# Performance work log

Measured on AMD Instinct MI355X. Metric: run time of the kernel, lower is better.

Reference implementation:

```python
import jax, jax.numpy as jnp
import numpy as np

B, CIN, T, H, W = 2, 256, 16, 16, 8
FF, COUT, NHEADS = 512, 256, 8
TEMP = 16.0
BN_EPS = 1e-5


def setup_inputs() -> dict:
    key = jax.random.key(0)
    ks = jax.random.split(key, 6)
    s_in = 1.0 / np.sqrt(CIN)
    s_ff = 1.0 / np.sqrt(FF)
    return {
        "x": jax.random.normal(ks[0], (B, CIN, T, H, W), jnp.float32),
        "WK": jax.random.uniform(ks[1], (FF, CIN), jnp.float32, -s_in, s_in),
        "WQ": jax.random.uniform(ks[2], (FF, CIN), jnp.float32, -s_in, s_in),
        "WV": jax.random.uniform(ks[3], (FF, CIN), jnp.float32, -s_in, s_in),
        "Wo": jax.random.uniform(ks[4], (COUT, FF), jnp.float32, -s_ff, s_ff),
        "bo": jax.random.uniform(ks[5], (COUT,), jnp.float32, -s_ff, s_ff),
        "gamma": jnp.ones((COUT,), jnp.float32),
        "beta": jnp.zeros((COUT,), jnp.float32),
    }


def reference(x, WK, WQ, WV, Wo, bo, gamma, beta):
    N = T * H * W
    xf = x.reshape(B, CIN, N)  # 1x1 conv3d == channel matmul
    dh = FF // NHEADS
    K = jnp.einsum("fc,bcn->bfn", WK, xf).reshape(B, NHEADS, dh, N)
    Q = jnp.einsum("fc,bcn->bfn", WQ, xf).reshape(B, NHEADS, dh, N)
    V = jnp.einsum("fc,bcn->bfn", WV, xf).reshape(B, NHEADS, dh, N)
    # KQ[b,h,i,j] = K_i . Q_j  (i = key token, j = query token, as in torch)
    KQ = jnp.einsum("bhdi,bhdj->bhij", K, Q) / TEMP
    # block-causal mask: token time index t = token_idx // (H*W); tril -> allow i >= j
    t_idx = jnp.arange(N) // (H * W)
    allow = t_idx[:, None] >= t_idx[None, :]  # (N, N)
    KQ = jnp.where(allow[None, None], KQ, -jnp.inf)
    attn = jax.nn.softmax(KQ, axis=3)  # softmax over j (last dim), as in torch
    # out[b,h,d,i] = sum_j V[b,h,d,j] * attn[b,h,i,j]
    Vo = jnp.einsum("bhdj,bhij->bhdi", V, attn).reshape(B, FF, N)
    y = jnp.einsum("of,bfn->bon", Wo, Vo) + bo[None, :, None]
    y = jax.nn.relu(y).reshape(B, COUT, T, H, W)
    out = x + y  # skip: out_dim == in_dim
    # BatchNorm3d (training-mode batch stats, biased var)
    mean = out.mean(axis=(0, 2, 3, 4), keepdims=True)
    var = out.var(axis=(0, 2, 3, 4), keepdims=True)
    norm = (out - mean) * jax.lax.rsqrt(var + BN_EPS)
    return norm * gamma[None, :, None, None, None] + beta[None, :, None, None, None]
```

## Files before the change

kernel.cpp:

```cpp
#include <hip/hip_runtime.h>
#include <math.h>

#define BB_   2
#define CIN_  256
#define NTOK_ 2048
#define FF_   512
#define COUT_ 256
#define NH_   8
#define DH_   64
#define HW_   128
#define BNEPS_ 1e-5f
#define SCALE_LOG2_ 0.09016844005556021f

typedef __attribute__((ext_vector_type(8))) short short8;
typedef __attribute__((ext_vector_type(4))) short bfx4;
typedef __attribute__((ext_vector_type(4))) float f32x4;

#if __has_builtin(__builtin_amdgcn_mfma_f32_16x16x16_bf16)
#define MFMA16(a, b, c) __builtin_amdgcn_mfma_f32_16x16x16_bf16(a, b, c, 0, 0, 0)
#else
#define MFMA16(a, b, c) __builtin_amdgcn_mfma_f32_16x16x16bf16_1k(a, b, c, 0, 0, 0)
#endif

__device__ inline unsigned short f2bf(float f) {
  union { float f; unsigned u; } v; v.f = f;
  unsigned r = (v.u + 0x7FFF + ((v.u >> 16) & 1)) >> 16;
  return (unsigned short)r;
}

__device__ __forceinline__ void dma16(const unsigned short* g, unsigned short* l) {
  __builtin_amdgcn_global_load_lds(
      (const __attribute__((address_space(1))) void*)g,
      (__attribute__((address_space(3))) void*)l, 16, 0, 0);
}

__global__ __launch_bounds__(256) void prep_kernel(
    const float* __restrict__ x, const float* __restrict__ WK,
    const float* __restrict__ WQ, const float* __restrict__ WV,
    const float* __restrict__ Wo, unsigned short* __restrict__ xT,
    unsigned short* __restrict__ Wkb, unsigned short* __restrict__ Wqb,
    unsigned short* __restrict__ Wvb, unsigned short* __restrict__ Wob) {
  __shared__ float T[64 * 65];
  const int tid = threadIdx.x;
  const int bid = blockIdx.x;
  if (bid < 256) {
    const int b = bid >> 7;
    const int rem = bid & 127;
    const int n0 = (rem >> 2) * 64;
    const int c0 = (rem & 3) * 64;
#pragma unroll
    for (int p = 0; p < 4; ++p) {
      const int idx = tid + 256 * p;
      const int row = idx >> 4, col = (idx & 15) * 4;
      const float4 v =
          *(const float4*)(x + (size_t)(b * CIN_ + c0 + row) * NTOK_ + n0 + col);
      T[row * 65 + col + 0] = v.x; T[row * 65 + col + 1] = v.y;
      T[row * 65 + col + 2] = v.z; T[row * 65 + col + 3] = v.w;
    }
    __syncthreads();
#pragma unroll
    for (int p = 0; p < 2; ++p) {
      const int idx = tid + 256 * p;
      const int nl = idx >> 3, c8 = (idx & 7) * 8;
      unsigned short u[8];
#pragma unroll
      for (int i = 0; i < 8; ++i) u[i] = f2bf(T[(c8 + i) * 65 + nl]);
      *(uint4*)(xT + ((size_t)(b * NTOK_ + n0 + nl)) * CIN_ + c0 + c8) =
          *(uint4*)u;
    }
  } else {
    const int t = bid - 256;
    const int which = t >> 5, blk = t & 31;
    const float* src = which == 0 ? WK : which == 1 ? WQ : which == 2 ? WV : Wo;
    unsigned short* dst = which == 0 ? Wkb : which == 1 ? Wqb : which == 2 ? Wvb : Wob;
    const int base = blk * 4096 + tid * 16;
#pragma unroll
    for (int p = 0; p < 4; ++p) {
      const float4 v = *(const float4*)(src + base + p * 4);
      ushort4 u;
      u.x = f2bf(v.x); u.y = f2bf(v.y); u.z = f2bf(v.z); u.w = f2bf(v.w);
      *(ushort4*)(dst + base + p * 4) = u;
    }
  }
}

__global__ __launch_bounds__(256, 3) void qkv_kernel(
    const unsigned short* __restrict__ xT, const unsigned short* __restrict__ Wkb,
    const unsigned short* __restrict__ Wqb, const unsigned short* __restrict__ Wvb,
    unsigned short* __restrict__ Kb, unsigned short* __restrict__ Qb,
    unsigned short* __restrict__ Vt) {
  __shared__ unsigned short Wsh[128 * 72];
  __shared__ unsigned short Xsh[64 * 72];
  const int tid = threadIdx.x;
  const int lane = tid & 63, w = tid >> 6;
  const int lx = lane & 15, q = lane >> 4;
  const int wm = w >> 1, wn = w & 1;
  const int n0 = blockIdx.x * 64;
  const int f0 = blockIdx.y * 128;
  const int b = blockIdx.z / 3, which = blockIdx.z % 3;
  const unsigned short* Wb = which == 0 ? Wkb : which == 1 ? Wqb : Wvb;

  const int srow = tid >> 3;
  const int soff = (tid & 7) * 8;
  const unsigned short* Wg = Wb + (size_t)(f0 + srow) * CIN_ + soff;
  const unsigned short* Xg = xT + ((size_t)(b * NTOK_ + n0 + srow)) * CIN_ + soff;

  uint4 wr[4], xr[2];
#pragma unroll
  for (int r = 0; r < 4; ++r) wr[r] = *(const uint4*)(Wg + (size_t)(32 * r) * CIN_);
#pragma unroll
  for (int r = 0; r < 2; ++r) xr[r] = *(const uint4*)(Xg + (size_t)(32 * r) * CIN_);

  f32x4 acc[4][2];
#pragma unroll
  for (int i = 0; i < 4; ++i)
#pragma unroll
    for (int j = 0; j < 2; ++j) acc[i][j] = (f32x4){0.f, 0.f, 0.f, 0.f};

  for (int kk = 0; kk < 4; ++kk) {
    __syncthreads();
#pragma unroll
    for (int r = 0; r < 4; ++r) *(uint4*)(Wsh + (srow + 32 * r) * 72 + soff) = wr[r];
#pragma unroll
    for (int r = 0; r < 2; ++r) *(uint4*)(Xsh + (srow + 32 * r) * 72 + soff) = xr[r];
    if (kk < 3) {
      const int c0 = (kk + 1) * 64;
#pragma unroll
      for (int r = 0; r < 4; ++r) wr[r] = *(const uint4*)(Wg + (size_t)(32 * r) * CIN_ + c0);
#pragma unroll
      for (int r = 0; r < 2; ++r) xr[r] = *(const uint4*)(Xg + (size_t)(32 * r) * CIN_ + c0);
    }
    __syncthreads();
    short8 xF[2][2];
#pragma unroll
    for (int i = 0; i < 2; ++i) {
      xF[i][0] = *(const short8*)(Xsh + (32 * wn + 16 * i + lx) * 72 + q * 8);
      xF[i][1] = *(const short8*)(Xsh + (32 * wn + 16 * i + lx) * 72 + 32 + q * 8);
    }
    if (which < 2) {
#pragma unroll
      for (int i = 0; i < 4; ++i) {
        const short8 w0 = *(const short8*)(Wsh + (64 * wm + 16 * i + lx) * 72 + q * 8);
        const short8 w1 = *(const short8*)(Wsh + (64 * wm + 16 * i + lx) * 72 + 32 + q * 8);
#pragma unroll
        for (int j = 0; j < 2; ++j) {
          acc[i][j] = __builtin_amdgcn_mfma_f32_16x16x32_bf16(w0, xF[j][0], acc[i][j], 0, 0, 0);
          acc[i][j] = __builtin_amdgcn_mfma_f32_16x16x32_bf16(w1, xF[j][1], acc[i][j], 0, 0, 0);
        }
      }
    } else {
#pragma unroll
      for (int jf = 0; jf < 4; ++jf) {
        const short8 w0 = *(const short8*)(Wsh + (64 * wm + 16 * jf + lx) * 72 + q * 8);
        const short8 w1 = *(const short8*)(Wsh + (64 * wm + 16 * jf + lx) * 72 + 32 + q * 8);
#pragma unroll
        for (int i = 0; i < 2; ++i) {
          acc[jf][i] = __builtin_amdgcn_mfma_f32_16x16x32_bf16(xF[i][0], w0, acc[jf][i], 0, 0, 0);
          acc[jf][i] = __builtin_amdgcn_mfma_f32_16x16x32_bf16(xF[i][1], w1, acc[jf][i], 0, 0, 0);
        }
      }
    }
  }

  __syncthreads();

  if (which < 2) {
    const float sc = (which == 0) ? SCALE_LOG2_ : 1.0f;
#pragma unroll
    for (int i = 0; i < 4; ++i)
#pragma unroll
      for (int j = 0; j < 2; ++j) {
        const int row = wm * 64 + 32 * wn + 16 * j + lx;
        const int d0 = 16 * i + 4 * q;
        ushort4 u;
        u.x = f2bf(acc[i][j][0] * sc); u.y = f2bf(acc[i][j][1] * sc);
        u.z = f2bf(acc[i][j][2] * sc); u.w = f2bf(acc[i][j][3] * sc);
        *(ushort4*)(Wsh + row * 72 + d0) = u;
      }
  } else {
#pragma unroll
    for (int jf = 0; jf < 4; ++jf)
#pragma unroll
      for (int i = 0; i < 2; ++i) {
        const int row = wm * 64 + 16 * jf + lx;
        const int nc = 32 * wn + 16 * i + 4 * q;
        ushort4 u;
        u.x = f2bf(acc[jf][i][0]); u.y = f2bf(acc[jf][i][1]);
        u.z = f2bf(acc[jf][i][2]); u.w = f2bf(acc[jf][i][3]);
        *(ushort4*)(Wsh + row * 72 + nc) = u;
      }
  }
  __syncthreads();

  const int h0 = f0 >> 6;
  if (which < 2) {
    unsigned short* Y = (which == 0 ? Kb : Qb);
#pragma unroll
    for (int p = 0; p < 4; ++p) {
      const int idx = tid + 256 * p;
      const int row = idx >> 3;
      const int c = (idx & 7) * 8;
      const uint4 val = *(const uint4*)(Wsh + row * 72 + c);
      *(uint4*)(Y + ((size_t)((b * NH_ + h0 + (row >> 6)) * NTOK_ + n0 + (row & 63))) * DH_ + c) = val;
    }
  } else {
#pragma unroll
    for (int p = 0; p < 4; ++p) {
      const int idx = tid + 256 * p;
      const int row = idx >> 3;
      const int c = (idx & 7) * 8;
      const uint4 val = *(const uint4*)(Wsh + row * 72 + c);
      *(uint4*)(Vt + ((size_t)((b * NH_ + h0 + (row >> 6)) * DH_ + (row & 63))) * NTOK_ + n0 + c) = val;
    }
  }
}

__global__ __launch_bounds__(256, 2) void attn_kernel(
    const unsigned short* __restrict__ Kb, const unsigned short* __restrict__ Qb,
    const unsigned short* __restrict__ Vt, unsigned short* __restrict__ Ob) {
  __shared__ __align__(16) unsigned short Qbuf[2][8192];
  __shared__ __align__(16) unsigned short Vbuf[2][8192];

  const int tid = threadIdx.x;
  const int lane = tid & 63;
  const int w = tid >> 6;
  const int lx = lane & 15;
  const int g = lane >> 4;

  const int bid = blockIdx.x;
  const int xcd = bid & 7;
  const int k = bid >> 3;
  const int bh = xcd * 2 + (k & 1);
  const int u = k >> 1;
  const int iblk = (u < 16) ? (31 - u) : (u - 16);
  const int h = bh & 7, b = bh >> 3;
  const int i0 = iblk * 64;
  const int njt = (iblk >> 1) + 1;

  const size_t bhs = (size_t)b * NH_ + h;
  const unsigned short* Kg = Kb + bhs * (size_t)NTOK_ * DH_ + (size_t)i0 * DH_;
  const unsigned short* Qg = Qb + bhs * (size_t)NTOK_ * DH_;
  const unsigned short* Vg = Vt + bhs * (size_t)DH_ * NTOK_;

  auto stage = [&](int buf, int j0) {
#pragma unroll
    for (int cc = 0; cc < 4; ++cc) {
      const int chunk = 4 * w + cc;
      {
        const int row = chunk * 8 + (lane >> 3);
        const int grp = (lane & 7) ^ (row & 7);
        dma16(Qg + (size_t)(j0 + row) * DH_ + grp * 8, &Qbuf[buf][chunk * 512]);
      }
      {
        const int row = chunk * 4 + (lane >> 4);
        const int grp = (lane & 15) ^ (row & 7);
        dma16(Vg + (size_t)row * NTOK_ + j0 + grp * 8, &Vbuf[buf][chunk * 512]);
      }
    }
  };

  const short8 aK0 = *(const short8*)(Kg + (16 * w + lx) * DH_ + g * 8);
  const short8 aK1 = *(const short8*)(Kg + (16 * w + lx) * DH_ + 32 + g * 8);

  f32x4 o[4];
#pragma unroll
  for (int t = 0; t < 4; ++t) o[t] = (f32x4){0.f, 0.f, 0.f, 0.f};
  float rs = 0.f;

  const int fr0 = ((g ^ (lx & 7)) << 3);
  const int fr1 = (((4 + g) ^ (lx & 7)) << 3);

  stage(0, 0);
  __syncthreads();

  int cur = 0;
  for (int jt = 0; jt < njt; ++jt) {
    if (jt + 1 < njt) stage(cur ^ 1, (jt + 1) * 128);

    const unsigned short* Qs = Qbuf[cur];
    const unsigned short* Vs = Vbuf[cur];

    f32x4 sa[8];
#pragma unroll
    for (int s = 0; s < 8; ++s) {
      const int row = 16 * s + lx;
      const short8 a0 = *(const short8*)(Qs + row * 64 + fr0);
      const short8 a1 = *(const short8*)(Qs + row * 64 + fr1);
      sa[s] = (f32x4){0.f, 0.f, 0.f, 0.f};
      sa[s] = __builtin_amdgcn_mfma_f32_16x16x32_bf16(a0, aK0, sa[s], 0, 0, 0);
      sa[s] = __builtin_amdgcn_mfma_f32_16x16x32_bf16(a1, aK1, sa[s], 0, 0, 0);
    }

#pragma unroll
    for (int s = 0; s < 8; ++s) {
      const float p0 = __builtin_amdgcn_exp2f(sa[s][0]);
      const float p1 = __builtin_amdgcn_exp2f(sa[s][1]);
      const float p2 = __builtin_amdgcn_exp2f(sa[s][2]);
      const float p3 = __builtin_amdgcn_exp2f(sa[s][3]);
      rs += (p0 + p1) + (p2 + p3);
      union { unsigned u[2]; bfx4 v; } pk;
      pk.u[0] = (__builtin_bit_cast(unsigned, p0) >> 16) |
                (__builtin_bit_cast(unsigned, p1) & 0xFFFF0000u);
      pk.u[1] = (__builtin_bit_cast(unsigned, p2) >> 16) |
                (__builtin_bit_cast(unsigned, p3) & 0xFFFF0000u);
      const int jgrp = 2 * s + (g >> 1);
      const int joff = (g & 1) << 2;
#pragma unroll
      for (int t = 0; t < 4; ++t) {
        const int row = 16 * t + lx;
        const bfx4 va = *(const bfx4*)(Vs + row * 128 +
                                       ((jgrp ^ (row & 7)) << 3) + joff);
        o[t] = MFMA16(va, pk.v, o[t]);
      }
    }

    __syncthreads();
    cur ^= 1;
  }

  rs += __shfl_xor(rs, 16);
  rs += __shfl_xor(rs, 32);
  const float invl = 1.0f / rs;
  const int n = i0 + 16 * w + lx;
#pragma unroll
  for (int t = 0; t < 4; ++t) {
    ushort4 uo;
    uo.x = f2bf(o[t][0] * invl); uo.y = f2bf(o[t][1] * invl);
    uo.z = f2bf(o[t][2] * invl); uo.w = f2bf(o[t][3] * invl);
    *(ushort4*)(Ob + ((size_t)(b * NTOK_ + n)) * FF_ + h * 64 + 16 * t + 4 * g) = uo;
  }
}

__global__ __launch_bounds__(256, 2) void proj_kernel(
    const unsigned short* __restrict__ Ob, const unsigned short* __restrict__ Wob,
    const float* __restrict__ bo, const float* __restrict__ x,
    float* __restrict__ pre) {
  __shared__ unsigned short Osh[32 * 72];
  __shared__ unsigned short Wsh[64 * 72];
  const int tid = threadIdx.x;
  const int lane = tid & 63, w = tid >> 6;
  const int lx = lane & 15, q = lane >> 4;
  const int n0 = blockIdx.x * 32;
  const int o0 = blockIdx.y * 64;
  const int b = blockIdx.z;

  const int srow = tid >> 3;
  const int soff = (tid & 7) * 8;
  const unsigned short* Og = Ob + ((size_t)(b * NTOK_ + n0 + srow)) * FF_ + soff;
  const unsigned short* Wg = Wob + (size_t)(o0 + srow) * FF_ + soff;

  uint4 orr, wrr[2];
  orr = *(const uint4*)(Og);
#pragma unroll
  for (int r = 0; r < 2; ++r) wrr[r] = *(const uint4*)(Wg + (size_t)(32 * r) * FF_);

  f32x4 acc[2];
#pragma unroll
  for (int i = 0; i < 2; ++i) acc[i] = (f32x4){0.f, 0.f, 0.f, 0.f};

  for (int kk = 0; kk < 8; ++kk) {
    __syncthreads();
    *(uint4*)(Osh + srow * 72 + soff) = orr;
#pragma unroll
    for (int r = 0; r < 2; ++r)
      *(uint4*)(Wsh + (srow + 32 * r) * 72 + soff) = wrr[r];
    if (kk < 7) {
      const int c0 = (kk + 1) * 64;
      orr = *(const uint4*)(Og + c0);
#pragma unroll
      for (int r = 0; r < 2; ++r)
        wrr[r] = *(const uint4*)(Wg + (size_t)(32 * r) * FF_ + c0);
    }
    __syncthreads();
    short8 aF[2][2], bF[2];
#pragma unroll
    for (int i = 0; i < 2; ++i) {
      aF[i][0] = *(const short8*)(Osh + (16 * i + lx) * 72 + q * 8);
      aF[i][1] = *(const short8*)(Osh + (16 * i + lx) * 72 + 32 + q * 8);
    }
    bF[0] = *(const short8*)(Wsh + (16 * w + lx) * 72 + q * 8);
    bF[1] = *(const short8*)(Wsh + (16 * w + lx) * 72 + 32 + q * 8);
#pragma unroll
    for (int i = 0; i < 2; ++i) {
      acc[i] = __builtin_amdgcn_mfma_f32_16x16x32_bf16(aF[i][0], bF[0], acc[i], 0, 0, 0);
      acc[i] = __builtin_amdgcn_mfma_f32_16x16x32_bf16(aF[i][1], bF[1], acc[i], 0, 0, 0);
    }
  }

  const int o = o0 + 16 * w + lx;
  const float bias = bo[o];
#pragma unroll
  for (int i = 0; i < 2; ++i) {
    const int n = n0 + 16 * i + 4 * q;
    const float4 xv = *(const float4*)(x + ((size_t)(b * CIN_ + o)) * NTOK_ + n);
    float4 v;
    v.x = fmaxf(acc[i][0] + bias, 0.f) + xv.x;
    v.y = fmaxf(acc[i][1] + bias, 0.f) + xv.y;
    v.z = fmaxf(acc[i][2] + bias, 0.f) + xv.z;
    v.w = fmaxf(acc[i][3] + bias, 0.f) + xv.w;
    *(float4*)(pre + ((size_t)(b * COUT_ + o)) * NTOK_ + n) = v;
  }
}

__global__ __launch_bounds__(512) void bn_kernel(
    float* __restrict__ out, const float* __restrict__ gamma,
    const float* __restrict__ beta) {
  __shared__ float red[16];
  const int c = blockIdx.x;
  const int tid = threadIdx.x;
  const int lane = tid & 63, w = tid >> 6;

  float4 v[2];
  float s = 0.f, s2 = 0.f;
#pragma unroll
  for (int b = 0; b < BB_; ++b) {
    float* base = out + ((size_t)(b * COUT_ + c)) * NTOK_;
    const float4 t = *(const float4*)(base + 4 * tid);
    v[b] = t;
    s += t.x + t.y + t.z + t.w;
    s2 += t.x * t.x + t.y * t.y + t.z * t.z + t.w * t.w;
  }
#pragma unroll
  for (int off = 32; off >= 1; off >>= 1) {
    s += __shfl_xor(s, off);
    s2 += __shfl_xor(s2, off);
  }
  if (lane == 0) { red[w] = s; red[8 + w] = s2; }
  __syncthreads();
  float S = 0.f, S2 = 0.f;
#pragma unroll
  for (int i = 0; i < 8; ++i) { S += red[i]; S2 += red[8 + i]; }
  const float inv = 1.0f / (float)(BB_ * NTOK_);
  const float mean = S * inv;
  const float var = S2 * inv - mean * mean;
  const float sc = rsqrtf(var + BNEPS_) * gamma[c];
  const float bt = beta[c];
#pragma unroll
  for (int b = 0; b < BB_; ++b) {
    float* base = out + ((size_t)(b * COUT_ + c)) * NTOK_;
    float4 t = v[b];
    t.x = (t.x - mean) * sc + bt;
    t.y = (t.y - mean) * sc + bt;
    t.z = (t.z - mean) * sc + bt;
    t.w = (t.w - mean) * sc + bt;
    *(float4*)(base + 4 * tid) = t;
  }
}

extern "C" void kernel_launch(void* const* d_in, const int* in_sizes, int n_in,
                              void* d_out, int out_size, void* d_ws, size_t ws_size,
                              hipStream_t stream) {
  (void)in_sizes; (void)n_in; (void)out_size; (void)ws_size;
  const float* x = (const float*)d_in[0];
  const float* WK = (const float*)d_in[1];
  const float* WQ = (const float*)d_in[2];
  const float* WV = (const float*)d_in[3];
  const float* Wo = (const float*)d_in[4];
  const float* bo = (const float*)d_in[5];
  const float* gamma = (const float*)d_in[6];
  const float* beta = (const float*)d_in[7];

  char* ws = (char*)d_ws;
  unsigned short* xT  = (unsigned short*)(ws);
  unsigned short* Wkb = (unsigned short*)(ws + 2097152);
  unsigned short* Wqb = (unsigned short*)(ws + 2359296);
  unsigned short* Wvb = (unsigned short*)(ws + 2621440);
  unsigned short* Wob = (unsigned short*)(ws + 2883584);
  unsigned short* Kb  = (unsigned short*)(ws + 3145728);
  unsigned short* Qb  = (unsigned short*)(ws + 7340032);
  unsigned short* Vt  = (unsigned short*)(ws + 11534336);
  unsigned short* Ob  = (unsigned short*)(ws + 15728640);
  float* out = (float*)d_out;

  prep_kernel<<<384, 256, 0, stream>>>(x, WK, WQ, WV, Wo, xT, Wkb, Wqb, Wvb, Wob);
  qkv_kernel<<<dim3(32, 4, 6), 256, 0, stream>>>(xT, Wkb, Wqb, Wvb, Kb, Qb, Vt);
  attn_kernel<<<dim3(512, 1, 1), 256, 0, stream>>>(Kb, Qb, Vt, Ob);
  proj_kernel<<<dim3(64, 4, 2), 256, 0, stream>>>(Ob, Wob, bo, x, out);
  bn_kernel<<<256, 512, 0, stream>>>(out, gamma, beta);
}
```

Before: 137.3 us.

## Fuse fp32-to-bf16 conversion and transpose into qkv and proj kernels

Removes the separate prep kernel that transposed x and converted weights to bf16. The qkv kernel now loads fp32 x and weights directly, transposes x through a shared-memory tile and converts both to bf16 while staging into LDS. The proj kernel likewise converts Wo from fp32 on the fly. This saves one launch and the round-trip of the bf16 copies through global memory. In exchange, x and the weights are re-read and re-converted by every block that uses them, there is an extra barrier per k-step, and LDS use per block grows.

```diff
diff --git a/kernel.cpp b/kernel.cpp
--- a/kernel.cpp
+++ b/kernel.cpp
@@ -34,63 +34,14 @@
       (__attribute__((address_space(3))) void*)l, 16, 0, 0);
 }
 
-__global__ __launch_bounds__(256) void prep_kernel(
+__global__ __launch_bounds__(256, 3) void qkv_kernel(
     const float* __restrict__ x, const float* __restrict__ WK,
     const float* __restrict__ WQ, const float* __restrict__ WV,
-    const float* __restrict__ Wo, unsigned short* __restrict__ xT,
-    unsigned short* __restrict__ Wkb, unsigned short* __restrict__ Wqb,
-    unsigned short* __restrict__ Wvb, unsigned short* __restrict__ Wob) {
-  __shared__ float T[64 * 65];
-  const int tid = threadIdx.x;
-  const int bid = blockIdx.x;
-  if (bid < 256) {
-    const int b = bid >> 7;
-    const int rem = bid & 127;
-    const int n0 = (rem >> 2) * 64;
-    const int c0 = (rem & 3) * 64;
-#pragma unroll
-    for (int p = 0; p < 4; ++p) {
-      const int idx = tid + 256 * p;
-      const int row = idx >> 4, col = (idx & 15) * 4;
-      const float4 v =
-          *(const float4*)(x + (size_t)(b * CIN_ + c0 + row) * NTOK_ + n0 + col);
-      T[row * 65 + col + 0] = v.x; T[row * 65 + col + 1] = v.y;
-      T[row * 65 + col + 2] = v.z; T[row * 65 + col + 3] = v.w;
-    }
-    __syncthreads();
-#pragma unroll
-    for (int p = 0; p < 2; ++p) {
-      const int idx = tid + 256 * p;
-      const int nl = idx >> 3, c8 = (idx & 7) * 8;
-      unsigned short u[8];
-#pragma unroll
-      for (int i = 0; i < 8; ++i) u[i] = f2bf(T[(c8 + i) * 65 + nl]);
-      *(uint4*)(xT + ((size_t)(b * NTOK_ + n0 + nl)) * CIN_ + c0 + c8) =
-          *(uint4*)u;
-    }
-  } else {
-    const int t = bid - 256;
-    const int which = t >> 5, blk = t & 31;
-    const float* src = which == 0 ? WK : which == 1 ? WQ : which == 2 ? WV : Wo;
-    unsigned short* dst = which == 0 ? Wkb : which == 1 ? Wqb : which == 2 ? Wvb : Wob;
-    const int base = blk * 4096 + tid * 16;
-#pragma unroll
-    for (int p = 0; p < 4; ++p) {
-      const float4 v = *(const float4*)(src + base + p * 4);
-      ushort4 u;
-      u.x = f2bf(v.x); u.y = f2bf(v.y); u.z = f2bf(v.z); u.w = f2bf(v.w);
-      *(ushort4*)(dst + base + p * 4) = u;
-    }
-  }
-}
-
-__global__ __launch_bounds__(256, 3) void qkv_kernel(
-    const unsigned short* __restrict__ xT, const unsigned short* __restrict__ Wkb,
-    const unsigned short* __restrict__ Wqb, const unsigned short* __restrict__ Wvb,
     unsigned short* __restrict__ Kb, unsigned short* __restrict__ Qb,
     unsigned short* __restrict__ Vt) {
   __shared__ unsigned short Wsh[128 * 72];
   __shared__ unsigned short Xsh[64 * 72];
+  __shared__ float T[64 * 65];
   const int tid = threadIdx.x;
   const int lane = tid & 63, w = tid >> 6;
   const int lx = lane & 15, q = lane >> 4;
@@ -98,18 +49,23 @@
   const int n0 = blockIdx.x * 64;
   const int f0 = blockIdx.y * 128;
   const int b = blockIdx.z / 3, which = blockIdx.z % 3;
-  const unsigned short* Wb = which == 0 ? Wkb : which == 1 ? Wqb : Wvb;
+  const float* Wb = which == 0 ? WK : which == 1 ? WQ : WV;
 
   const int srow = tid >> 3;
   const int soff = (tid & 7) * 8;
-  const unsigned short* Wg = Wb + (size_t)(f0 + srow) * CIN_ + soff;
-  const unsigned short* Xg = xT + ((size_t)(b * NTOK_ + n0 + srow)) * CIN_ + soff;
-
-  uint4 wr[4], xr[2];
-#pragma unroll
-  for (int r = 0; r < 4; ++r) wr[r] = *(const uint4*)(Wg + (size_t)(32 * r) * CIN_);
-#pragma unroll
-  for (int r = 0; r < 2; ++r) xr[r] = *(const uint4*)(Xg + (size_t)(32 * r) * CIN_);
+  const float* Wg = Wb + (size_t)(f0 + srow) * CIN_ + soff;
+  const int tc = tid >> 4;
+  const int tn = (tid & 15) * 4;
+
+  float4 wr[4][2], xr[4];
+#pragma unroll
+  for (int r = 0; r < 4; ++r) {
+    wr[r][0] = *(const float4*)(Wg + (size_t)(32 * r) * CIN_);
+    wr[r][1] = *(const float4*)(Wg + (size_t)(32 * r) * CIN_ + 4);
+  }
+#pragma unroll
+  for (int p = 0; p < 4; ++p)
+    xr[p] = *(const float4*)(x + (size_t)(b * CIN_ + tc + 16 * p) * NTOK_ + n0 + tn);
 
   f32x4 acc[4][2];
 #pragma unroll
@@ -120,15 +76,40 @@
   for (int kk = 0; kk < 4; ++kk) {
     __syncthreads();
 #pragma unroll
-    for (int r = 0; r < 4; ++r) *(uint4*)(Wsh + (srow + 32 * r) * 72 + soff) = wr[r];
-#pragma unroll
-    for (int r = 0; r < 2; ++r) *(uint4*)(Xsh + (srow + 32 * r) * 72 + soff) = xr[r];
+    for (int p = 0; p < 4; ++p) {
+      const int row = tc + 16 * p;
+      T[row * 65 + tn + 0] = xr[p].x; T[row * 65 + tn + 1] = xr[p].y;
+      T[row * 65 + tn + 2] = xr[p].z; T[row * 65 + tn + 3] = xr[p].w;
+    }
+#pragma unroll
+    for (int r = 0; r < 4; ++r) {
+      unsigned short u[8];
+      u[0] = f2bf(wr[r][0].x); u[1] = f2bf(wr[r][0].y);
+      u[2] = f2bf(wr[r][0].z); u[3] = f2bf(wr[r][0].w);
+      u[4] = f2bf(wr[r][1].x); u[5] = f2bf(wr[r][1].y);
+      u[6] = f2bf(wr[r][1].z); u[7] = f2bf(wr[r][1].w);
+      *(uint4*)(Wsh + (srow + 32 * r) * 72 + soff) = *(uint4*)u;
+    }
+    __syncthreads();
+#pragma unroll
+    for (int p = 0; p < 2; ++p) {
+      const int idx = tid + 256 * p;
+      const int nl = idx >> 3, c8 = (idx & 7) * 8;
+      unsigned short u[8];
+#pragma unroll
+      for (int i = 0; i < 8; ++i) u[i] = f2bf(T[(c8 + i) * 65 + nl]);
+      *(uint4*)(Xsh + nl * 72 + c8) = *(uint4*)u;
+    }
     if (kk < 3) {
       const int c0 = (kk + 1) * 64;
 #pragma unroll
-      for (int r = 0; r < 4; ++r) wr[r] = *(const uint4*)(Wg + (size_t)(32 * r) * CIN_ + c0);
-#pragma unroll
-      for (int r = 0; r < 2; ++r) xr[r] = *(const uint4*)(Xg + (size_t)(32 * r) * CIN_ + c0);
+      for (int r = 0; r < 4; ++r) {
+        wr[r][0] = *(const float4*)(Wg + (size_t)(32 * r) * CIN_ + c0);
+        wr[r][1] = *(const float4*)(Wg + (size_t)(32 * r) * CIN_ + c0 + 4);
+      }
+#pragma unroll
+      for (int p = 0; p < 4; ++p)
+        xr[p] = *(const float4*)(x + (size_t)(b * CIN_ + c0 + tc + 16 * p) * NTOK_ + n0 + tn);
     }
     __syncthreads();
     short8 xF[2][2];
@@ -332,7 +313,7 @@
 }
 
 __global__ __launch_bounds__(256, 2) void proj_kernel(
-    const unsigned short* __restrict__ Ob, const unsigned short* __restrict__ Wob,
+    const unsigned short* __restrict__ Ob, const float* __restrict__ Wo,
     const float* __restrict__ bo, const float* __restrict__ x,
     float* __restrict__ pre) {
   __shared__ unsigned short Osh[32 * 72];
@@ -347,12 +328,16 @@
   const int srow = tid >> 3;
   const int soff = (tid & 7) * 8;
   const unsigned short* Og = Ob + ((size_t)(b * NTOK_ + n0 + srow)) * FF_ + soff;
-  const unsigned short* Wg = Wob + (size_t)(o0 + srow) * FF_ + soff;
-
-  uint4 orr, wrr[2];
+  const float* Wg = Wo + (size_t)(o0 + srow) * FF_ + soff;
+
+  uint4 orr;
+  float4 wrr[2][2];
   orr = *(const uint4*)(Og);
 #pragma unroll
-  for (int r = 0; r < 2; ++r) wrr[r] = *(const uint4*)(Wg + (size_t)(32 * r) * FF_);
+  for (int r = 0; r < 2; ++r) {
+    wrr[r][0] = *(const float4*)(Wg + (size_t)(32 * r) * FF_);
+    wrr[r][1] = *(const float4*)(Wg + (size_t)(32 * r) * FF_ + 4);
+  }
 
   f32x4 acc[2];
 #pragma unroll
@@ -362,14 +347,22 @@
     __syncthreads();
     *(uint4*)(Osh + srow * 72 + soff) = orr;
 #pragma unroll
-    for (int r = 0; r < 2; ++r)
-      *(uint4*)(Wsh + (srow + 32 * r) * 72 + soff) = wrr[r];
+    for (int r = 0; r < 2; ++r) {
+      unsigned short u[8];
+      u[0] = f2bf(wrr[r][0].x); u[1] = f2bf(wrr[r][0].y);
+      u[2] = f2bf(wrr[r][0].z); u[3] = f2bf(wrr[r][0].w);
+      u[4] = f2bf(wrr[r][1].x); u[5] = f2bf(wrr[r][1].y);
+      u[6] = f2bf(wrr[r][1].z); u[7] = f2bf(wrr[r][1].w);
+      *(uint4*)(Wsh + (srow + 32 * r) * 72 + soff) = *(uint4*)u;
+    }
     if (kk < 7) {
       const int c0 = (kk + 1) * 64;
       orr = *(const uint4*)(Og + c0);
 #pragma unroll
-      for (int r = 0; r < 2; ++r)
-        wrr[r] = *(const uint4*)(Wg + (size_t)(32 * r) * FF_ + c0);
+      for (int r = 0; r < 2; ++r) {
+        wrr[r][0] = *(const float4*)(Wg + (size_t)(32 * r) * FF_ + c0);
+        wrr[r][1] = *(const float4*)(Wg + (size_t)(32 * r) * FF_ + c0 + 4);
+      }
     }
     __syncthreads();
     short8 aF[2][2], bF[2];
@@ -461,20 +454,14 @@
   const float* beta = (const float*)d_in[7];
 
   char* ws = (char*)d_ws;
-  unsigned short* xT  = (unsigned short*)(ws);
-  unsigned short* Wkb = (unsigned short*)(ws + 2097152);
-  unsigned short* Wqb = (unsigned short*)(ws + 2359296);
-  unsigned short* Wvb = (unsigned short*)(ws + 2621440);
-  unsigned short* Wob = (unsigned short*)(ws + 2883584);
   unsigned short* Kb  = (unsigned short*)(ws + 3145728);
   unsigned short* Qb  = (unsigned short*)(ws + 7340032);
   unsigned short* Vt  = (unsigned short*)(ws + 11534336);
   unsigned short* Ob  = (unsigned short*)(ws + 15728640);
   float* out = (float*)d_out;
 
-  prep_kernel<<<384, 256, 0, stream>>>(x, WK, WQ, WV, Wo, xT, Wkb, Wqb, Wvb, Wob);
-  qkv_kernel<<<dim3(32, 4, 6), 256, 0, stream>>>(xT, Wkb, Wqb, Wvb, Kb, Qb, Vt);
+  qkv_kernel<<<dim3(32, 4, 6), 256, 0, stream>>>(x, WK, WQ, WV, Kb, Qb, Vt);
   attn_kernel<<<dim3(512, 1, 1), 256, 0, stream>>>(Kb, Qb, Vt, Ob);
-  proj_kernel<<<dim3(64, 4, 2), 256, 0, stream>>>(Ob, Wob, bo, x, out);
+  proj_kernel<<<dim3(64, 4, 2), 256, 0, stream>>>(Ob, Wo, bo, x, out);
   bn_kernel<<<256, 512, 0, stream>>>(out, gamma, beta);
 }
```

Result: faster. 119.6 us (median of 2 runs) (-12.8%).
